# Optimization experiments

Hardware: AMD Instinct MI355X
Metric: run time of the kernel (lower is better)

## Reference

```python
import jax, jax.numpy as jnp
import numpy as np

B, T, F, D, H, DFF, L = 8, 1024, 64, 512, 8, 2048, 3
DH = D // H
PERIODS = np.array([16, 256, 4096], np.int32)
CMS_LRS = np.array([0.01, 0.001, 0.0001], np.float32)
TITANS_LR = 0.01
TITANS_CLIP = 0.1


def layernorm(x, w, b):
    m = x.mean(-1, keepdims=True)
    v = x.var(-1, keepdims=True)
    return (x - m) * jax.lax.rsqrt(v + 1e-5) * w + b


def setup_inputs() -> dict:
    key = jax.random.key(0)
    ks = jax.random.split(key, 40)
    f32 = jnp.float32
    def rn(i, shape, s=0.02):
        return jax.random.normal(ks[i], shape, f32) * s
    inp = {
        'x': jax.random.normal(ks[0], (B, T, F), f32),
        'titans_W': jnp.zeros((D, D), f32),
        'cms_summary': jnp.zeros((L, D), f32),
        'cms_buf_sum': jnp.zeros((L, D), f32),
        'cms_count': jnp.zeros((L,), jnp.int32),
        'cms_step': jnp.zeros((L,), jnp.int32),
        'in_norm_w': jnp.ones((F,), f32), 'in_norm_b': jnp.zeros((F,), f32),
        'in_proj_W': rn(1, (D, F)), 'in_proj_b': jnp.zeros((D,), f32),
        'W_base': rn(2, (D, D), 0.01),
        'tit_out_W': rn(3, (D, D)), 'tit_out_b': jnp.zeros((D,), f32),
        'gate_W': rn(4, (L, D, D)), 'gate_b': jnp.zeros((L, D), f32),
        'comb_W': rn(5, (D, L * D)), 'comb_b': jnp.zeros((D,), f32),
        'n1_w': jnp.ones((D,), f32), 'n1_b': jnp.zeros((D,), f32),
        'qkv_W': rn(6, (3 * D, D)), 'qkv_b': jnp.zeros((3 * D,), f32),
        'ao_W': rn(7, (D, D)), 'ao_b': jnp.zeros((D,), f32),
        'n2_w': jnp.ones((D,), f32), 'n2_b': jnp.zeros((D,), f32),
        'f1_W': rn(8, (DFF, D)), 'f1_b': jnp.zeros((DFF,), f32),
        'f2_W': rn(9, (D, DFF)), 'f2_b': jnp.zeros((D,), f32),
        'fn_w': jnp.ones((D,), f32), 'fn_b': jnp.zeros((D,), f32),
        'head_W': rn(10, (1, D)), 'head_b': jnp.zeros((1,), f32),
    }
    return inp


def cms_tick_all(means, summary, buf_sum, count, step, gate_W, gate_b):
    """Sequential tick over T timesteps, vectorized over the L levels.
    means: [T, D] batch-mean of final hidden at each timestep."""
    periods = jnp.asarray(PERIODS)
    lrs = jnp.asarray(CMS_LRS)
    def step_fn(carry, m):
        summ, bs, cnt, stp = carry
        bs = bs + m[None, :]              # [L, D]
        cnt = cnt + 1
        stp = stp + 1
        fire = cnt >= periods              # [L]
        acc = bs / cnt.astype(bs.dtype)[:, None]
        g = jax.nn.sigmoid(jnp.einsum('lij,lj->li', gate_W, acc) + gate_b)
        new_summ = jnp.where(fire[:, None], (1.0 - lrs)[:, None] * summ + lrs[:, None] * g * acc, summ)
        bs = jnp.where(fire[:, None], jnp.zeros_like(bs), bs)
        cnt = jnp.where(fire, jnp.zeros_like(cnt), cnt)
        return (new_summ, bs, cnt, stp), None
    (summary, buf_sum, count, step), _ = jax.lax.scan(step_fn, (summary, buf_sum, count, step), means)
    return summary, buf_sum, count, step


def reference(x, titans_W, cms_summary, cms_buf_sum, cms_count, cms_step,
              in_norm_w, in_norm_b, in_proj_W, in_proj_b,
              W_base, tit_out_W, tit_out_b,
              gate_W, gate_b, comb_W, comb_b,
              n1_w, n1_b, qkv_W, qkv_b, ao_W, ao_b,
              n2_w, n2_b, f1_W, f1_b, f2_W, f2_b,
              fn_w, fn_b, head_W, head_b):
    # input norm + projection: [B,T,F] -> [B,T,D]
    h = layernorm(x, in_norm_w, in_norm_b) @ in_proj_W.T + in_proj_b
    # Titans fast-weight read
    W = W_base + titans_W
    tit = (h @ W.T) @ tit_out_W.T + tit_out_b
    # Titans fast-weight update (detached in the original)
    hs = jax.lax.stop_gradient(h)
    target = hs.mean(axis=1)               # [B, D]
    query = hs[:, -1, :]                   # [B, D]
    pred_m = query @ titans_W.T
    err = (target - pred_m).mean(axis=0)   # [D]
    grad = jnp.outer(err, query.mean(axis=0))
    gn = jnp.linalg.norm(grad)
    grad = jnp.where(gn > TITANS_CLIP, grad * (TITANS_CLIP / gn), grad)
    new_W = titans_W + TITANS_LR * grad
    h = h + tit
    # CMS residual from current summaries: concat [L*D] -> combine -> [D]
    cms_out = cms_summary.reshape(L * D) @ comb_W.T + comb_b
    h = h + cms_out                        # broadcast over [B,T,D]
    # transformer block (pre-norm, causal MHA)
    hn = layernorm(h, n1_w, n1_b)
    qkv = hn @ qkv_W.T + qkv_b
    q, k, v = jnp.split(qkv, 3, axis=-1)
    def to_heads(t):
        return t.reshape(B, T, H, DH).transpose(0, 2, 1, 3)
    q, k, v = to_heads(q), to_heads(k), to_heads(v)
    scores = jnp.einsum('bhqd,bhkd->bhqk', q, k) / np.sqrt(DH).astype(np.float32)
    causal = jnp.triu(jnp.ones((T, T), bool), 1)
    scores = jnp.where(causal, -jnp.inf, scores)
    attn = jax.nn.softmax(scores, axis=-1)
    ao = jnp.einsum('bhqk,bhkd->bhqd', attn, v).transpose(0, 2, 1, 3).reshape(B, T, D)
    h = h + ao @ ao_W.T + ao_b
    hn2 = layernorm(h, n2_w, n2_b)
    h = h + jax.nn.gelu(hn2 @ f1_W.T + f1_b, approximate=False) @ f2_W.T + f2_b
    h = layernorm(h, fn_w, fn_b)
    pred = (h @ head_W.T + head_b).squeeze(-1)   # [B, T]
    # CMS tick over all T steps (detached in the original)
    means = jax.lax.stop_gradient(h).mean(axis=0)  # [T, D]
    ns, nb, nc, nt = cms_tick_all(means, cms_summary, cms_buf_sum, cms_count, cms_step, gate_W, gate_b)
    return pred, new_W, ns, nb, nc, nt
```

## Files before the change

### kernel.cpp

```cpp
#include <hip/hip_runtime.h>
#include <hip/hip_bf16.h>
#include <math.h>

#define Bdim 8
#define Tdim 1024
#define Fdim 64
#define Ddim 512
#define Lcms 3

#define OFF_PRED 0
#define OFF_W    8192
#define OFF_NS   270336
#define OFF_NB   271872
#define OFF_NC   273408
#define OFF_NT   273411

typedef __hip_bfloat16 bf16;
typedef __attribute__((ext_vector_type(8))) short s8;
typedef __attribute__((ext_vector_type(4))) float f4;

__device__ __forceinline__ float b2f(bf16 v){ return __bfloat162float(v); }
__device__ __forceinline__ bf16  f2b(float v){ return __float2bfloat16(v); }
__device__ __forceinline__ short fb16(float v){ bf16 t = __float2bfloat16(v); return *reinterpret_cast<short*>(&t); }
__device__ __forceinline__ float sh2f(short s){ bf16 t = *reinterpret_cast<bf16*>(&s); return __bfloat162float(t); }
__device__ __forceinline__ float toF(float v){ return v; }
__device__ __forceinline__ float toF(bf16 v){ return __bfloat162float(v); }
template<typename T> __device__ __forceinline__ T fromF(float v);
template<> __device__ __forceinline__ float fromF<float>(float v){ return v; }
template<> __device__ __forceinline__ bf16  fromF<bf16 >(float v){ return f2b(v); }

__device__ __forceinline__ f4 mfma16(s8 a, s8 b, f4 c){
  return __builtin_amdgcn_mfma_f32_16x16x32_bf16(a, b, c, 0, 0, 0);
}

__device__ __forceinline__ void gload16(const bf16* g, bf16* l){
  __builtin_amdgcn_global_load_lds(
      (const __attribute__((address_space(1))) unsigned*)g,
      (__attribute__((address_space(3))) unsigned*)l, 16, 0, 0);
}

__device__ __forceinline__ float gelu_fast(float x){
  float z2 = 1.5957691216f*(x + 0.044715f*x*x*x);
  z2 = fminf(fmaxf(z2, -18.f), 18.f);
  return x / (1.f + __expf(-z2));
}

template<typename TW>
__device__ __forceinline__ void front_misc(int blk, int tid,
    const TW* x, const TW* nw, const TW* nb_, bf16* xn,
    const TW* Wbse, const TW* tW, bf16* Wout,
    const TW* summ, const TW* combW, const TW* combb, float* outv){
  if (blk < 2048){
    int row = blk*4 + (tid>>6);
    int lane = tid & 63;
    float v = toF(x[(size_t)row*Fdim + lane]);
    float s = v, s2 = v*v;
    #pragma unroll
    for (int off=32; off; off>>=1){ s += __shfl_down(s,off); s2 += __shfl_down(s2,off); }
    s = __shfl(s, 0); s2 = __shfl(s2, 0);
    float mu = s*(1.f/64.f);
    float var = s2*(1.f/64.f) - mu*mu;
    float rstd = rsqrtf(var + 1e-5f);
    xn[(size_t)row*Fdim + lane] = f2b((v-mu)*rstd*toF(nw[lane]) + toF(nb_[lane]));
  } else if (blk < 3072){
    int i = (blk-2048)*256 + tid;
    Wout[i] = f2b(toF(Wbse[i]) + toF(tW[i]));
  } else {
    __shared__ float s_s[Lcms*Ddim];
    for (int i=tid;i<Lcms*Ddim;i+=256) s_s[i] = toF(summ[i]);
    __syncthreads();
    int wave = tid>>6, lane = tid&63;
    int d = (blk-3072)*4 + wave;
    const TW* wr = combW + (size_t)d*(Lcms*Ddim);
    float a = 0.f;
    for (int j=lane;j<Lcms*Ddim;j+=64) a += s_s[j]*toF(wr[j]);
    #pragma unroll
    for (int off=32; off; off>>=1) a += __shfl_down(a,off);
    if (lane==0) outv[d] = a + toF(combb[d]);
  }
}
__global__ __launch_bounds__(256) void k_front(
    const void* s0, const void* s1, const void* s2, const void* s3,
    const void* s4, const void* s5, const void* s6, const void* s7,
    const void* s8v, const void* s9, const void* s10, const void* s11,
    const void* s12, const void* s13,
    bf16* __restrict__ dst, const unsigned* __restrict__ w1, int* __restrict__ flag,
    const int* __restrict__ cnt, int* __restrict__ params,
    const void* x, const void* nw, const void* nb_, bf16* xn,
    const void* Wbse, const void* tW, bf16* Wout,
    const void* summ, const void* combW, const void* combb, float* outv,
    float* __restrict__ colsum){
  bool isbf = (w1[0] == 0x3F803F80u);
  int blk = blockIdx.x, tid = threadIdx.x;
  if (blk==0 && tid==0){
    flag[0] = isbf ? 1 : 0;
    const int P[3] = {16,256,4096};
    for (int l=0;l<3;l++){
      int c0 = cnt[l];
      int t1 = P[l] - c0 - 1; if (t1 < 0) t1 = 0;
      int K = (t1 >= Tdim) ? 0 : 1 + (Tdim-1-t1)/P[l];
      params[l*4+0]=t1; params[l*4+1]=K; params[l*4+2]=c0+t1+1; params[l*4+3]=c0;
    }
  }
  if (blk == 1){
    for (int i=tid; i<Bdim*Ddim; i+=256) colsum[i] = 0.f;
  }
  if (blk < 1024){
    const void* srcs[14] = {s0,s1,s2,s3,s4,s5,s6,s7,s8v,s9,s10,s11,s12,s13};
    const int   ns[14]   = {262144,512,786432,1536,262144,512,1048576,2048,1048576,512,
                            32768,512,786432,1536};
    const int gstride = 1024*256;
    int gid = blk*256 + tid;
    int base = 0;
    #pragma unroll
    for (int s=0;s<14;s++){
      int n = ns[s];
      if (isbf){
        const short* sp = (const short*)srcs[s]; short* dp = (short*)(dst+base);
        for (int i=gid;i<n;i+=gstride) dp[i] = sp[i];
      } else {
        const float* sp = (const float*)srcs[s];
        for (int i=gid;i<n;i+=gstride) dst[base+i] = f2b(sp[i]);
      }
      base += n;
    }
  } else {
    int b2 = blk - 1024;
    if (isbf) front_misc<bf16>(b2, tid, (const bf16*)x,(const bf16*)nw,(const bf16*)nb_,xn,
                               (const bf16*)Wbse,(const bf16*)tW,Wout,
                               (const bf16*)summ,(const bf16*)combW,(const bf16*)combb,outv);
    else      front_misc<float>(b2, tid, (const float*)x,(const float*)nw,(const float*)nb_,xn,
                               (const float*)Wbse,(const float*)tW,Wout,
                               (const float*)summ,(const float*)combW,(const float*)combb,outv);
  }
}

template<typename TW>
__device__ __forceinline__ void titans_err_impl(const bf16* h, const float* colsum,
    const TW* tW, float* err, float* qmean){
  int wave = threadIdx.x>>6, lane = threadIdx.x&63;
  int d = blockIdx.x*4 + wave;
  const TW* wr = tW + (size_t)d*Ddim;
  float s = 0.f;
  #pragma unroll
  for (int b=0;b<Bdim;b++){
    const bf16* q = h + ((size_t)b*Tdim + (Tdim-1))*Ddim;
    float p = 0.f;
    for (int j=lane;j<Ddim;j+=64) p += b2f(q[j])*toF(wr[j]);
    s += p;
  }
  #pragma unroll
  for (int off=32; off; off>>=1) s += __shfl_down(s,off);
  if (lane==0){
    float e=0.f, qm=0.f;
    #pragma unroll
    for (int b=0;b<Bdim;b++){
      e  += colsum[b*Ddim+d]*(1.f/(float)Tdim);
      qm += b2f(h[((size_t)b*Tdim + (Tdim-1))*Ddim + d]);
    }
    err[d]   = (e - s)*(1.f/(float)Bdim);
    qmean[d] = qm*(1.f/(float)Bdim);
  }
}
__global__ __launch_bounds__(256) void k_titans_err(const bf16* h, const float* colsum,
    const void* tW, float* err, float* qmean, const int* flg){
  if (*flg) titans_err_impl<bf16>(h,colsum,(const bf16*)tW,err,qmean);
  else      titans_err_impl<float>(h,colsum,(const float*)tW,err,qmean);
}

template<typename TW>
__device__ __forceinline__ void new_W_impl(const TW* tW, const float* err, const float* qmean,
    TW* outW){
  int tid = threadIdx.x;
  float a = err[tid]*err[tid] + err[tid+256]*err[tid+256];
  float b = qmean[tid]*qmean[tid] + qmean[tid+256]*qmean[tid+256];
  #pragma unroll
  for (int off=32; off; off>>=1){ a += __shfl_down(a,off); b += __shfl_down(b,off); }
  __shared__ float sa[4], sb[4];
  int lane = tid & 63, wid = tid >> 6;
  if (lane==0){ sa[wid]=a; sb[wid]=b; }
  __syncthreads();
  float A = sa[0]+sa[1]+sa[2]+sa[3];
  float Bq= sb[0]+sb[1]+sb[2]+sb[3];
  float gn = sqrtf(A*Bq);
  float sf = 0.01f * (gn > 0.1f ? 0.1f/gn : 1.0f);
  int i = blockIdx.x*256 + tid;
  int r = i >> 9, c = i & 511;
  outW[i] = fromF<TW>(toF(tW[i]) + sf*err[r]*qmean[c]);
}
__global__ __launch_bounds__(256) void k_new_W(const void* tW, const float* err,
    const float* qmean, void* out, const int* flg){
  if (*flg) new_W_impl<bf16>((const bf16*)tW, err, qmean, ((bf16*)out)+OFF_W);
  else      new_W_impl<float>((const float*)tW, err, qmean, ((float*)out)+OFF_W);
}

template<int MODE, int DEPTH>
__global__ __launch_bounds__(512) void gemm_mfma(const bf16* __restrict__ A,
    const bf16* __restrict__ Bw, const bf16* __restrict__ bias,
    const float* __restrict__ colvec, bf16* __restrict__ Cout,
    const bf16* __restrict__ resid, int M, int N, int K, float* __restrict__ colsum){
  __shared__ __align__(16) bf16 As[DEPTH][128*32];
  __shared__ __align__(16) bf16 Bs[DEPTH][128*32];
  int tid = threadIdx.x, wave = tid>>6, lane = tid&63, quad = lane>>4, l16 = lane&15;
  int row0 = blockIdx.x*128, col0 = blockIdx.y*128;
  int wr = (wave>>2)*64, wc = (wave&3)*32;
  int srow = wave*16 + (lane>>2);
  int scol = (((lane&3) ^ ((lane>>3)&3)))*8;
  int rswz = (quad ^ ((l16>>1)&3))*8;
  f4 acc[8] = {};
  int niter = K >> 5;
  #define STAGE(bu, k0) { \
    gload16(A  + (size_t)(row0 + srow)*K + (k0) + scol, &As[bu][wave*512 + lane*8]); \
    gload16(Bw + (size_t)(col0 + srow)*K + (k0) + scol, &Bs[bu][wave*512 + lane*8]); \
  }
  STAGE(0, 0)
  if (DEPTH >= 3 && niter > 1) STAGE(1, 32)
  if (DEPTH >= 4 && niter > 2) STAGE(2, 64)
  for (int k=0; k<niter; k++){
    int bu = k & (DEPTH-1);
    if (DEPTH == 2){
      if (k+1 < niter){
        STAGE((k+1)&1, (k+1)<<5)
        asm volatile("s_waitcnt vmcnt(2)" ::: "memory");
      } else {
        asm volatile("s_waitcnt vmcnt(0)" ::: "memory");
      }
    } else {
      if (k+3 < niter){
        STAGE((k+3)&3, (k+3)<<5)
        asm volatile("s_waitcnt vmcnt(6)" ::: "memory");
      } else if (k+2 < niter){
        asm volatile("s_waitcnt vmcnt(4)" ::: "memory");
      } else if (k+1 < niter){
        asm volatile("s_waitcnt vmcnt(2)" ::: "memory");
      } else {
        asm volatile("s_waitcnt vmcnt(0)" ::: "memory");
      }
    }
    __builtin_amdgcn_s_barrier();
    s8 af[4], bfv[2];
    #pragma unroll
    for (int i=0;i<4;i++) af[i]  = *reinterpret_cast<const s8*>(&As[bu][(wr + i*16 + l16)*32 + rswz]);
    #pragma unroll
    for (int j=0;j<2;j++) bfv[j] = *reinterpret_cast<const s8*>(&Bs[bu][(wc + j*16 + l16)*32 + rswz]);
    #pragma unroll
    for (int i=0;i<4;i++)
      #pragma unroll
      for (int j=0;j<2;j++)
        acc[i*2+j] = mfma16(af[i], bfv[j], acc[i*2+j]);
    asm volatile("s_waitcnt lgkmcnt(0)" ::: "memory");
    __builtin_amdgcn_s_barrier();
  }
  #undef STAGE
  float cs[2] = {0.f, 0.f};
  #pragma unroll
  for (int i=0;i<4;i++){
    #pragma unroll
    for (int j=0;j<2;j++){
      int n = col0 + wc + j*16 + l16;
      f4 a = acc[i*2+j];
      #pragma unroll
      for (int r=0;r<4;r++){
        int m = row0 + wr + i*16 + quad*4 + r;
        float v = a[r];
        if (MODE & 1) v += b2f(bias[n]);
        if (MODE & 8) v += colvec[n];
        if (MODE & 4) v = gelu_fast(v);
        if (MODE & 2) v += b2f(resid[(size_t)m*Ddim + n]);
        Cout[(size_t)m*N + n] = f2b(v);
        if (MODE & 16) cs[j] += v;
      }
    }
  }
  if (MODE & 16){
    int bIdx = blockIdx.x >> 3;
    #pragma unroll
    for (int j=0;j<2;j++){
      float c = cs[j];
      c += __shfl_xor(c, 16);
      c += __shfl_xor(c, 32);
      if (quad == 0)
        atomicAdd(&colsum[bIdx*Ddim + col0 + wc + j*16 + l16], c);
    }
  }
}

template<int MODE>
__global__ __launch_bounds__(512) void gemm_mfma64(const bf16* __restrict__ A,
    const bf16* __restrict__ Bw, const bf16* __restrict__ bias,
    const float* __restrict__ colvec, bf16* __restrict__ Cout,
    const bf16* __restrict__ resid, int M, int N, int K){
  __shared__ __align__(16) bf16 As[2][64*32];
  __shared__ __align__(16) bf16 Bs[2][128*32];
  int tid = threadIdx.x, wave = tid>>6, lane = tid&63, quad = lane>>4, l16 = lane&15;
  int row0 = blockIdx.x*64, col0 = blockIdx.y*128;
  int wr = (wave>>2)*32, wc = (wave&3)*32;
  int srow = lane>>2;
  int scol = (((lane&3) ^ ((lane>>3)&3)))*8;
  int rswz = (quad ^ ((l16>>1)&3))*8;
  f4 acc[4] = {};
  int niter = K >> 5;
  #define STAGE64(bu, k0) { \
    if (wave < 4) \
      gload16(A + (size_t)(row0 + wave*16 + srow)*K + (k0) + scol, &As[bu][wave*512 + lane*8]); \
    gload16(Bw + (size_t)(col0 + wave*16 + srow)*K + (k0) + scol, &Bs[bu][wave*512 + lane*8]); \
  }
  STAGE64(0, 0)
  for (int k=0; k<niter; k++){
    int bu = k & 1;
    if (k+1 < niter){
      STAGE64((k+1)&1, (k+1)<<5)
      if (wave < 4) asm volatile("s_waitcnt vmcnt(2)" ::: "memory");
      else          asm volatile("s_waitcnt vmcnt(1)" ::: "memory");
    } else {
      asm volatile("s_waitcnt vmcnt(0)" ::: "memory");
    }
    __builtin_amdgcn_s_barrier();
    s8 af[2], bfv[2];
    #pragma unroll
    for (int i=0;i<2;i++) af[i]  = *reinterpret_cast<const s8*>(&As[bu][(wr + i*16 + l16)*32 + rswz]);
    #pragma unroll
    for (int j=0;j<2;j++) bfv[j] = *reinterpret_cast<const s8*>(&Bs[bu][(wc + j*16 + l16)*32 + rswz]);
    #pragma unroll
    for (int i=0;i<2;i++)
      #pragma unroll
      for (int j=0;j<2;j++)
        acc[i*2+j] = mfma16(af[i], bfv[j], acc[i*2+j]);
    asm volatile("s_waitcnt lgkmcnt(0)" ::: "memory");
    __builtin_amdgcn_s_barrier();
  }
  #undef STAGE64
  #pragma unroll
  for (int i=0;i<2;i++){
    #pragma unroll
    for (int j=0;j<2;j++){
      int n = col0 + wc + j*16 + l16;
      f4 a = acc[i*2+j];
      #pragma unroll
      for (int r=0;r<4;r++){
        int m = row0 + wr + i*16 + quad*4 + r;
        float v = a[r];
        if (MODE & 1) v += b2f(bias[n]);
        if (MODE & 8) v += colvec[n];
        if (MODE & 4) v = gelu_fast(v);
        if (MODE & 2) v += b2f(resid[(size_t)m*Ddim + n]);
        Cout[(size_t)m*N + n] = f2b(v);
      }
    }
  }
}

template<typename TW>
__device__ __forceinline__ void ln_impl(const bf16* in, const TW* w, const TW* b, bf16* outp){
  int row = blockIdx.x;
  const bf16* r = in + (size_t)row*Ddim;
  int tid = threadIdx.x;
  float v0 = b2f(r[tid]), v1 = b2f(r[tid + 256]);
  float s = v0+v1, s2 = v0*v0 + v1*v1;
  #pragma unroll
  for (int off=32; off; off>>=1){ s += __shfl_down(s,off); s2 += __shfl_down(s2,off); }
  __shared__ float sa[4], sb[4];
  int lane = tid & 63, wid = tid >> 6;
  if (lane==0){ sa[wid]=s; sb[wid]=s2; }
  __syncthreads();
  float ts  = sa[0]+sa[1]+sa[2]+sa[3];
  float ts2 = sb[0]+sb[1]+sb[2]+sb[3];
  float mu = ts*(1.f/(float)Ddim);
  float var = ts2*(1.f/(float)Ddim) - mu*mu;
  float rstd = rsqrtf(var + 1e-5f);
  outp[(size_t)row*Ddim + tid]       = f2b((v0-mu)*rstd*toF(w[tid])     + toF(b[tid]));
  outp[(size_t)row*Ddim + tid + 256] = f2b((v1-mu)*rstd*toF(w[tid+256]) + toF(b[tid+256]));
}
__global__ __launch_bounds__(256) void k_ln(const bf16* in, const void* w, const void* b,
    bf16* outp, const int* flg){
  if (*flg) ln_impl<bf16>(in,(const bf16*)w,(const bf16*)b,outp);
  else      ln_impl<float>(in,(const float*)w,(const float*)b,outp);
}

template<typename TW>
__device__ __forceinline__ void ln_hm_impl(const bf16* in, const TW* w, const TW* b,
    bf16* outp, const TW* hw, const TW* hb, TW* pred, float* means){
  int t = blockIdx.x;
  int tid = threadIdx.x, wave = tid>>6, lane = tid&63;
  int d0 = lane*8;
  __shared__ float msum[4][Ddim];
  float wv[8], bv[8], hwv[8];
  #pragma unroll
  for (int j=0;j<8;j++){ wv[j]=toF(w[d0+j]); bv[j]=toF(b[d0+j]); hwv[j]=toF(hw[d0+j]); }
  float hb0 = toF(hb[0]);
  float osum[8] = {0,0,0,0,0,0,0,0};
  #pragma unroll
  for (int rr=0; rr<2; rr++){
    int bb = wave*2 + rr;
    size_t row = (size_t)bb*Tdim + t;
    s8 raw = *reinterpret_cast<const s8*>(in + row*Ddim + d0);
    float v[8];
    float s=0.f, s2=0.f;
    #pragma unroll
    for (int j=0;j<8;j++){ v[j]=sh2f(raw[j]); s+=v[j]; s2+=v[j]*v[j]; }
    #pragma unroll
    for (int off=32; off; off>>=1){ s += __shfl_down(s,off); s2 += __shfl_down(s2,off); }
    s = __shfl(s,0); s2 = __shfl(s2,0);
    float mu = s*(1.f/(float)Ddim);
    float var = s2*(1.f/(float)Ddim) - mu*mu;
    float rstd = rsqrtf(var + 1e-5f);
    float sp = 0.f;
    s8 ob;
    #pragma unroll
    for (int j=0;j<8;j++){
      float o = (v[j]-mu)*rstd*wv[j] + bv[j];
      ob[j] = fb16(o);
      sp += o*hwv[j];
      osum[j] += o;
    }
    *reinterpret_cast<s8*>(outp + row*Ddim + d0) = ob;
    #pragma unroll
    for (int off=32; off; off>>=1) sp += __shfl_down(sp,off);
    if (lane==0) pred[row] = fromF<TW>(sp + hb0);
  }
  #pragma unroll
  for (int j=0;j<8;j++) msum[wave][d0+j] = osum[j];
  __syncthreads();
  for (int d=tid; d<Ddim; d+=256)
    means[(size_t)t*Ddim + d] = (msum[0][d]+msum[1][d]+msum[2][d]+msum[3][d])*(1.f/8.f);
}
__global__ __launch_bounds__(256) void k_ln_hm(const bf16* in, const void* w, const void* b,
    bf16* outp, const void* hw, const void* hb, void* out, float* means, const int* flg){
  if (*flg) ln_hm_impl<bf16>(in,(const bf16*)w,(const bf16*)b,outp,
                             (const bf16*)hw,(const bf16*)hb,((bf16*)out)+OFF_PRED,means);
  else      ln_hm_impl<float>(in,(const float*)w,(const float*)b,outp,
                             (const float*)hw,(const float*)hb,((float*)out)+OFF_PRED,means);
}

__global__ __launch_bounds__(256) void k_attn_mfma(const bf16* __restrict__ qkv,
                                                   bf16* __restrict__ ao){
  int blk = blockIdx.x;
  int bh = blk & 63;
  int qt = 15 - (blk >> 6);
  int head = bh & 7, b = bh >> 3;
  __shared__ __align__(16) bf16 Ks[2][64][72];
  __shared__ __align__(16) unsigned Vt4[2][64*36];
  __shared__ __align__(16) bf16 Ps[4][16][72];
  int tid = threadIdx.x, wave = tid>>6, lane = tid&63, quad = lane>>4, l16 = lane&15;
  int q0w = qt*64 + wave*16;
  const bf16* basep = qkv + (size_t)b*Tdim*1536 + head*64;
  s8 qf0 = *reinterpret_cast<const s8*>(basep + (size_t)(q0w+l16)*1536 + quad*8);
  s8 qf1 = *reinterpret_cast<const s8*>(basep + (size_t)(q0w+l16)*1536 + 32 + quad*8);
  f4 o[4] = {{0,0,0,0},{0,0,0,0},{0,0,0,0},{0,0,0,0}};
  float m_r[4] = {-3.0e38f,-3.0e38f,-3.0e38f,-3.0e38f};
  float l_r[4] = {0.f,0.f,0.f,0.f};
  int key_s = tid>>3, dgk = (tid&7)*8;
  int vp = tid>>3, dgv = (tid&7)*8;
  int vu4 = (((vp>>2) ^ (tid&7)) & 7)*4 + (vp&3);
  int nch = qt + 1;
  s8 kr0[2], kr1[2], vra[2], vrb[2];
  {
    const bf16* kp = basep + (size_t)key_s*1536 + 512 + dgk;
    kr0[0] = *reinterpret_cast<const s8*>(kp);
    kr1[0] = *reinterpret_cast<const s8*>(kp + (size_t)32*1536);
    const bf16* vpa = basep + (size_t)(2*vp)*1536 + 1024 + dgv;
    vra[0] = *reinterpret_cast<const s8*>(vpa);
    vrb[0] = *reinterpret_cast<const s8*>(vpa + 1536);
    if (1 < nch){
      const bf16* kp1 = basep + (size_t)(64+key_s)*1536 + 512 + dgk;
      kr0[1] = *reinterpret_cast<const s8*>(kp1);
      kr1[1] = *reinterpret_cast<const s8*>(kp1 + (size_t)32*1536);
      const bf16* vpa1 = basep + (size_t)(64 + 2*vp)*1536 + 1024 + dgv;
      vra[1] = *reinterpret_cast<const s8*>(vpa1);
      vrb[1] = *reinterpret_cast<const s8*>(vpa1 + 1536);
    }
  }
  auto do_chunk = [&](int ch, int bu){
    f4 sc4[4] = {{0,0,0,0},{0,0,0,0},{0,0,0,0},{0,0,0,0}};
    #pragma unroll
    for (int t=0;t<4;t++){
      sc4[t] = mfma16(qf0, *reinterpret_cast<const s8*>(&Ks[bu][t*16+l16][quad*8]),    sc4[t]);
      sc4[t] = mfma16(qf1, *reinterpret_cast<const s8*>(&Ks[bu][t*16+l16][32+quad*8]), sc4[t]);
    }
    int key0 = ch*64 + l16;
    #pragma unroll
    for (int r=0;r<4;r++){
      int qrow = q0w + quad*4 + r;
      float a0 = (key0      <= qrow) ? sc4[0][r]*0.125f : -3.0e38f;
      float a1 = (key0 + 16 <= qrow) ? sc4[1][r]*0.125f : -3.0e38f;
      float a2 = (key0 + 32 <= qrow) ? sc4[2][r]*0.125f : -3.0e38f;
      float a3 = (key0 + 48 <= qrow) ? sc4[3][r]*0.125f : -3.0e38f;
      float mx = fmaxf(fmaxf(a0,a1), fmaxf(a2,a3));
      mx = fmaxf(mx, __shfl_xor(mx,1)); mx = fmaxf(mx, __shfl_xor(mx,2));
      mx = fmaxf(mx, __shfl_xor(mx,4)); mx = fmaxf(mx, __shfl_xor(mx,8));
      float mnew = fmaxf(m_r[r], mx);
      float al = __expf(m_r[r]-mnew); m_r[r] = mnew;
      float p0 = __expf(a0-mnew), p1 = __expf(a1-mnew);
      float p2 = __expf(a2-mnew), p3 = __expf(a3-mnew);
      float rs = (p0+p1)+(p2+p3);
      rs += __shfl_xor(rs,1); rs += __shfl_xor(rs,2);
      rs += __shfl_xor(rs,4); rs += __shfl_xor(rs,8);
      l_r[r] = l_r[r]*al + rs;
      o[0][r]*=al; o[1][r]*=al; o[2][r]*=al; o[3][r]*=al;
      int prow = quad*4+r;
      *reinterpret_cast<short*>(&Ps[wave][prow][l16])    = fb16(p0);
      *reinterpret_cast<short*>(&Ps[wave][prow][16+l16]) = fb16(p1);
      *reinterpret_cast<short*>(&Ps[wave][prow][32+l16]) = fb16(p2);
      *reinterpret_cast<short*>(&Ps[wave][prow][48+l16]) = fb16(p3);
    }
    asm volatile("s_waitcnt lgkmcnt(0)" ::: "memory");
    s8 pf0 = *reinterpret_cast<const s8*>(&Ps[wave][l16][quad*8]);
    s8 pf1 = *reinterpret_cast<const s8*>(&Ps[wave][l16][32+quad*8]);
    #pragma unroll
    for (int j=0;j<4;j++){
      int d = j*16 + l16;
      int swz = (d>>3) & 7;
      s8 b0 = *reinterpret_cast<const s8*>(&Vt4[bu][d*36 + ((quad   ^ swz))*4]);
      s8 b1 = *reinterpret_cast<const s8*>(&Vt4[bu][d*36 + (((4+quad)^ swz))*4]);
      o[j] = mfma16(pf0, b0, o[j]);
      o[j] = mfma16(pf1, b1, o[j]);
    }
  };
  for (int ch0=0; ch0<nch; ch0+=2){
    #pragma unroll
    for (int s=0;s<2;s++){
      if (ch0+s < nch){
        *reinterpret_cast<s8*>(&Ks[s][key_s][dgk])    = kr0[s];
        *reinterpret_cast<s8*>(&Ks[s][32+key_s][dgk]) = kr1[s];
        #pragma unroll
        for (int j=0;j<8;j++){
          unsigned w = (unsigned)(unsigned short)vra[s][j] | ((unsigned)(unsigned short)vrb[s][j] << 16);
          Vt4[s][(dgv+j)*36 + vu4] = w;
        }
      }
    }
    __syncthreads();
    #pragma unroll
    for (int s=0;s<2;s++){
      int chn = ch0 + 2 + s;
      if (chn < nch){
        const bf16* kp = basep + (size_t)(chn*64+key_s)*1536 + 512 + dgk;
        kr0[s] = *reinterpret_cast<const s8*>(kp);
        kr1[s] = *reinterpret_cast<const s8*>(kp + (size_t)32*1536);
        const bf16* vpa = basep + (size_t)(chn*64 + 2*vp)*1536 + 1024 + dgv;
        vra[s] = *reinterpret_cast<const s8*>(vpa);
        vrb[s] = *reinterpret_cast<const s8*>(vpa + 1536);
      }
    }
    do_chunk(ch0, 0);
    if (ch0+1 < nch) do_chunk(ch0+1, 1);
    if (ch0+2 < nch) __syncthreads();
  }
  #pragma unroll
  for (int r=0;r<4;r++){
    float inv = 1.f/l_r[r];
    size_t rowb = (size_t)(b*Tdim + q0w + quad*4 + r)*Ddim + head*64;
    ao[rowb + l16]      = f2b(o[0][r]*inv);
    ao[rowb + 16 + l16] = f2b(o[1][r]*inv);
    ao[rowb + 32 + l16] = f2b(o[2][r]*inv);
    ao[rowb + 48 + l16] = f2b(o[3][r]*inv);
  }
}

template<typename TW>
__device__ __forceinline__ void cms_acc_impl(const float* means, const TW* bs0,
    const int* params, float* acc, bf16* acch, float* tailtmp){
  int tid = threadIdx.x;
  if (blockIdx.x < 384){
    int l = blockIdx.x>>7, k = blockIdx.x&127;
    int K = params[l*4+1];
    if (k >= K){
      for (int d=tid; d<Ddim; d+=256) acch[((size_t)l*128+k)*Ddim + d] = f2b(0.f);
      return;
    }
    int t1 = params[l*4], cnt0 = params[l*4+2];
    const int P[3] = {16,256,4096};
    int lo = (k==0) ? 0 : t1 + (k-1)*P[l] + 1;
    int hi = t1 + k*P[l];
    float inv = 1.f/((k==0) ? (float)cnt0 : (float)P[l]);
    int lane = tid&63, strip = tid>>6;
    __shared__ float red[4][Ddim];
    float4 a0 = {0,0,0,0}, a1 = {0,0,0,0};
    for (int t=lo+strip; t<=hi; t+=4){
      const float4* row = (const float4*)(means + (size_t)t*Ddim);
      float4 v0 = row[lane], v1 = row[lane+64];
      a0.x+=v0.x; a0.y+=v0.y; a0.z+=v0.z; a0.w+=v0.w;
      a1.x+=v1.x; a1.y+=v1.y; a1.z+=v1.z; a1.w+=v1.w;
    }
    ((float4*)red[strip])[lane]    = a0;
    ((float4*)red[strip])[lane+64] = a1;
    __syncthreads();
    for (int d=tid; d<Ddim; d+=256){
      float s = red[0][d]+red[1][d]+red[2][d]+red[3][d];
      if (k==0) s += toF(bs0[l*Ddim+d]);
      float v = s*inv;
      acc[((size_t)l*65+k)*Ddim + d] = v;
      acch[((size_t)l*128+k)*Ddim + d] = f2b(v);
    }
  } else {
    int bb = blockIdx.x - 384;
    int l = bb>>5, chunk = bb&31;
    int t1 = params[l*4], K = params[l*4+1];
    const int P[3] = {16,256,4096};
    int lo = (K==0) ? 0 : t1 + (K-1)*P[l] + 1;
    int f = tid & 127, strip = tid >> 7;
    int tbeg = chunk*32, tend = tbeg + 32;
    if (tbeg < lo) tbeg = lo;
    float4 a = {0,0,0,0};
    for (int t=tbeg+strip; t<tend; t+=2){
      float4 v = ((const float4*)(means + (size_t)t*Ddim))[f];
      a.x+=v.x; a.y+=v.y; a.z+=v.z; a.w+=v.w;
    }
    __shared__ float4 redt[2][128];
    redt[strip][f] = a;
    __syncthreads();
    if (strip==0){
      float4 b = redt[1][f];
      a.x+=b.x; a.y+=b.y; a.z+=b.z; a.w+=b.w;
      ((float4*)(tailtmp + ((size_t)l*32 + chunk)*Ddim))[f] = a;
    }
  }
}
__global__ __launch_bounds__(256) void k_cms_acc(const float* means, const void* bs0,
    const int* params, float* acc, bf16* acch, float* tailtmp, const int* flg){
  if (*flg) cms_acc_impl<bf16>(means,(const bf16*)bs0,params,acc,acch,tailtmp);
  else      cms_acc_impl<float>(means,(const float*)bs0,params,acc,acch,tailtmp);
}

__global__ __launch_bounds__(256) void k_cms_gate_mfma(const bf16* __restrict__ accbh,
    const bf16* __restrict__ wg, const bf16* __restrict__ wgb, float* __restrict__ g){
  int l = blockIdx.y;
  const bf16* A  = accbh + (size_t)l*128*Ddim;
  const bf16* Bw = wg    + (size_t)l*Ddim*Ddim;
  __shared__ __align__(16) bf16 As[128*32];
  __shared__ __align__(16) bf16 Bs[128*32];
  int tid = threadIdx.x, wave = tid>>6, lane = tid&63, quad = lane>>4, l16 = lane&15;
  int col0 = blockIdx.x*128;
  int wr = (wave>>1)*64, wc = (wave&1)*64;
  int srow = lane>>2, scol = (lane&3)*8;
  f4 acc[16] = {};
  for (int k0=0; k0<Ddim; k0+=32){
    __syncthreads();
    #pragma unroll
    for (int it=0; it<2; it++){
      int c = wave*2 + it;
      gload16(A  + (size_t)(c*16 + srow)*Ddim + k0 + scol, &As[c*512 + lane*8]);
      gload16(Bw + (size_t)(col0 + c*16 + srow)*Ddim + k0 + scol, &Bs[c*512 + lane*8]);
    }
    __syncthreads();
    s8 af[4], bfv[4];
    #pragma unroll
    for (int i=0;i<4;i++) af[i]  = *reinterpret_cast<const s8*>(&As[(wr + i*16 + l16)*32 + quad*8]);
    #pragma unroll
    for (int j=0;j<4;j++) bfv[j] = *reinterpret_cast<const s8*>(&Bs[(wc + j*16 + l16)*32 + quad*8]);
    #pragma unroll
    for (int i=0;i<4;i++)
      #pragma unroll
      for (int j=0;j<4;j++)
        acc[i*4+j] = mfma16(af[i], bfv[j], acc[i*4+j]);
  }
  #pragma unroll
  for (int i=0;i<4;i++){
    #pragma unroll
    for (int j=0;j<4;j++){
      int n = col0 + wc + j*16 + l16;
      f4 a = acc[i*4+j];
      #pragma unroll
      for (int r=0;r<4;r++){
        int m = wr + i*16 + quad*4 + r;
        if (m < 65){
          float v = a[r] + b2f(wgb[l*Ddim + n]);
          g[((size_t)l*65 + m)*Ddim + n] = 1.f/(1.f + __expf(-v));
        }
      }
    }
  }
}

template<typename TW>
__device__ __forceinline__ void cms_final_impl(const float* acc, const float* g,
    const float* tailtmp, const TW* summ0, const TW* bs0, const int* params,
    const int* step0, TW* out){
  int l = blockIdx.x;
  int t1 = params[l*4], K = params[l*4+1], c0 = params[l*4+3];
  const int P[3] = {16,256,4096};
  const float LR[3] = {0.01f,0.001f,0.0001f};
  float lr = LR[l];
  for (int d=threadIdx.x; d<Ddim; d+=256){
    float s = toF(summ0[l*Ddim + d]);
    for (int k=0;k<K;k++)
      s = (1.f-lr)*s + lr*g[((size_t)l*65+k)*Ddim+d]*acc[((size_t)l*65+k)*Ddim+d];
    out[OFF_NS + l*Ddim + d] = fromF<TW>(s);
    float nbv = (K==0) ? toF(bs0[l*Ddim+d]) : 0.f;
    #pragma unroll
    for (int c=0;c<32;c++) nbv += tailtmp[((size_t)l*32+c)*Ddim + d];
    out[OFF_NB + l*Ddim + d] = fromF<TW>(nbv);
  }
  if (threadIdx.x==0){
    int nc = (K==0) ? c0 + Tdim : (Tdim-1 - (t1 + (K-1)*P[l]));
    out[OFF_NC + l] = fromF<TW>((float)nc);
    out[OFF_NT + l] = fromF<TW>((float)(step0[l] + Tdim));
  }
}
__global__ __launch_bounds__(256) void k_cms_final(const float* acc, const float* g,
    const float* tailtmp, const void* summ0, const void* bs0, const int* params,
    const int* step0, void* out, const int* flg){
  if (*flg) cms_final_impl<bf16>(acc,g,tailtmp,(const bf16*)summ0,(const bf16*)bs0,params,step0,(bf16*)out);
  else      cms_final_impl<float>(acc,g,tailtmp,(const float*)summ0,(const float*)bs0,params,step0,(float*)out);
}

extern "C" void kernel_launch(void* const* d_in, const int* in_sizes, int n_in,
                              void* d_out, int out_size, void* d_ws, size_t ws_size,
                              hipStream_t stream) {
  (void)in_sizes; (void)n_in; (void)out_size; (void)ws_size;
  const void* x           = d_in[0];
  const void* titansW     = d_in[1];
  const void* cms_summary = d_in[2];
  const void* cms_bufsum  = d_in[3];
  const int*  cms_count   = (const int*)d_in[4];
  const int*  cms_step    = (const int*)d_in[5];
  const void* in_norm_w   = d_in[6];
  const void* in_norm_b   = d_in[7];
  const void* in_proj_W   = d_in[8];
  const void* in_proj_b   = d_in[9];
  const void* W_base      = d_in[10];
  const void* tit_out_W   = d_in[11];
  const void* tit_out_b   = d_in[12];
  const void* gate_W      = d_in[13];
  const void* gate_b      = d_in[14];
  const void* comb_W      = d_in[15];
  const void* comb_b      = d_in[16];
  const void* n1_w        = d_in[17];
  const void* n1_b        = d_in[18];
  const void* qkv_W       = d_in[19];
  const void* qkv_b       = d_in[20];
  const void* ao_W        = d_in[21];
  const void* ao_b        = d_in[22];
  const void* n2_w        = d_in[23];
  const void* n2_b        = d_in[24];
  const void* f1_W        = d_in[25];
  const void* f1_b        = d_in[26];
  const void* f2_W        = d_in[27];
  const void* f2_b        = d_in[28];
  const void* fn_w        = d_in[29];
  const void* fn_b        = d_in[30];
  const void* head_W      = d_in[31];
  const void* head_b      = d_in[32];

  char* u8 = (char*)d_ws;
  bf16*  h     = (bf16*)(u8 + 0);
  bf16*  hnA   = (bf16*)(u8 + 8388608);
  bf16*  big   = (bf16*)(u8 + 16777216);
  bf16*  xn    = big;
  bf16*  tmid  = big + (size_t)8192*1536;
  float* means = (float*)(u8 + 50331648);
  bf16*  Wb    = (bf16*)(u8 + 52428800);
  bf16*  wall  = (bf16*)(u8 + 52953088);
  bf16*  wtit  = wall;
  bf16*  wtitb = wall + 262144;
  bf16*  wqkv  = wall + 262656;
  bf16*  wqkvb = wall + 1049088;
  bf16*  wao   = wall + 1050624;
  bf16*  waob  = wall + 1312768;
  bf16*  wf1   = wall + 1313280;
  bf16*  wf1b  = wall + 2361856;
  bf16*  wf2   = wall + 2363904;
  bf16*  wf2b  = wall + 3412480;
  bf16*  wproj = wall + 3412992;
  bf16*  wprojb= wall + 3445760;
  bf16*  wgate = wall + 3446272;
  bf16*  wgateb= wall + 4232704;
  float* errv  = (float*)(u8 + 61454336);
  float* qmean = (float*)(u8 + 61456384);
  float* cmsout= (float*)(u8 + 61458944);
  float* accb  = (float*)(u8 + 61460992);
  float* gbuf  = (float*)(u8 + 61860352);
  bf16*  accbh = (bf16*) (u8 + 62259712);
  int*   params= (int*)  (u8 + 62652928);
  int*   dflag = (int*)  (u8 + 62652992);
  float* colsum= (float*)(u8 + 62659584);
  float* tailtmp=(float*)(u8 + 63183872);

  k_front<<<4224, 256, 0, stream>>>(tit_out_W, tit_out_b, qkv_W, qkv_b, ao_W, ao_b,
                                    f1_W, f1_b, f2_W, f2_b, in_proj_W, in_proj_b,
                                    gate_W, gate_b, wall, (const unsigned*)in_norm_w,
                                    dflag, cms_count, params,
                                    x, in_norm_w, in_norm_b, xn,
                                    W_base, titansW, Wb,
                                    cms_summary, comb_W, comb_b, cmsout, colsum);
  gemm_mfma<17,2><<<dim3(64,4), 512, 0, stream>>>(xn, wproj, wprojb, nullptr, h, nullptr, 8192, 512, 64, colsum);
  k_titans_err<<<128, 256, 0, stream>>>(h, colsum, titansW, errv, qmean, dflag);
  k_new_W<<<1024, 256, 0, stream>>>(titansW, errv, qmean, d_out, dflag);
  gemm_mfma64<0><<<dim3(128,4), 512, 0, stream>>>(h, Wb, nullptr, nullptr, tmid, nullptr, 8192, 512, 512);
  gemm_mfma64<11><<<dim3(128,4), 512, 0, stream>>>(tmid, wtit, wtitb, cmsout, h, h, 8192, 512, 512);
  k_ln<<<8192, 256, 0, stream>>>(h, n1_w, n1_b, hnA, dflag);
  gemm_mfma<1,2><<<dim3(64,12), 512, 0, stream>>>(hnA, wqkv, wqkvb, nullptr, big, nullptr, 8192, 1536, 512, nullptr);
  k_attn_mfma<<<1024, 256, 0, stream>>>(big, tmid);
  gemm_mfma64<3><<<dim3(128,4), 512, 0, stream>>>(tmid, wao, waob, nullptr, h, h, 8192, 512, 512);
  k_ln<<<8192, 256, 0, stream>>>(h, n2_w, n2_b, hnA, dflag);
  gemm_mfma<5,2><<<dim3(64,16), 512, 0, stream>>>(hnA, wf1, wf1b, nullptr, big, nullptr, 8192, 2048, 512, nullptr);
  gemm_mfma64<3><<<dim3(128,4), 512, 0, stream>>>(big, wf2, wf2b, nullptr, h, h, 8192, 512, 2048);
  k_ln_hm<<<1024, 256, 0, stream>>>(h, fn_w, fn_b, hnA, head_W, head_b, d_out, means, dflag);
  k_cms_acc<<<480, 256, 0, stream>>>(means, cms_bufsum, params, accb, accbh, tailtmp, dflag);
  k_cms_gate_mfma<<<dim3(4,3), 256, 0, stream>>>(accbh, wgate, wgateb, gbuf);
  k_cms_final<<<Lcms, 256, 0, stream>>>(accb, gbuf, tailtmp, cms_summary, cms_bufsum, params, cms_step, d_out, dflag);
}
```

Before: 419.7 us.

## Fold LayerNorm into following GEMMs via row stats and precomputed weight vectors

Removes the two standalone LayerNorm kernels before the QKV and FFN1 GEMMs. The preceding residual GEMM epilogues now accumulate per-row sum and sum-of-squares with atomics. The LN gain is folded into the weight copies in k_front, which also precomputes the per-column vectors W·w and W·b+bias. The consuming GEMMs then apply the mean and rstd correction in their epilogue to the raw residual stream. This saves two full read/write passes over the activation tensor and two launches, at the cost of atomics, more work in k_front, and precision risk from the E[x²]-μ² variance formula applied to bf16-rounded values.

Measured after the change: 431.8 us. 2.9% more time.

```diff
diff --git a/kernel.cpp b/kernel.cpp
--- a/kernel.cpp
+++ b/kernel.cpp
@@ -49,7 +49,9 @@
 __device__ __forceinline__ void front_misc(int blk, int tid,
     const TW* x, const TW* nw, const TW* nb_, bf16* xn,
     const TW* Wbse, const TW* tW, bf16* Wout,
-    const TW* summ, const TW* combW, const TW* combb, float* outv){
+    const TW* summ, const TW* combW, const TW* combb, float* outv,
+    const TW* qkvW, const TW* qkvb, const TW* f1W, const TW* f1b,
+    const TW* n1w, const TW* n1b, const TW* n2w, const TW* n2b, float* cvec){
   if (blk < 2048){
     int row = blk*4 + (tid>>6);
     int lane = tid & 63;
@@ -65,7 +67,7 @@
   } else if (blk < 3072){
     int i = (blk-2048)*256 + tid;
     Wout[i] = f2b(toF(Wbse[i]) + toF(tW[i]));
-  } else {
+  } else if (blk < 3200){
     __shared__ float s_s[Lcms*Ddim];
     for (int i=tid;i<Lcms*Ddim;i+=256) s_s[i] = toF(summ[i]);
     __syncthreads();
@@ -77,6 +79,27 @@
     #pragma unroll
     for (int off=32; off; off>>=1) a += __shfl_down(a,off);
     if (lane==0) outv[d] = a + toF(combb[d]);
+  } else {
+    int wave = tid>>6, lane = tid&63;
+    int n = (blk-3200)*4 + wave;
+    const TW *wr, *lw, *lb; float bb; float *o1, *o2;
+    if (n < 1536){
+      wr = qkvW + (size_t)n*Ddim; lw = n1w; lb = n1b; bb = toF(qkvb[n]);
+      o1 = cvec + n; o2 = cvec + 1536 + n;
+    } else {
+      int m2 = n - 1536;
+      wr = f1W + (size_t)m2*Ddim; lw = n2w; lb = n2b; bb = toF(f1b[m2]);
+      o1 = cvec + 3072 + m2; o2 = cvec + 5120 + m2;
+    }
+    float a1 = 0.f, a2 = 0.f;
+    for (int j=lane;j<Ddim;j+=64){
+      float wv = toF(wr[j]);
+      a1 += wv*toF(lw[j]);
+      a2 += wv*toF(lb[j]);
+    }
+    #pragma unroll
+    for (int off=32; off; off>>=1){ a1 += __shfl_down(a1,off); a2 += __shfl_down(a2,off); }
+    if (lane==0){ *o1 = a1; *o2 = a2 + bb; }
   }
 }
 __global__ __launch_bounds__(256) void k_front(
@@ -89,7 +112,9 @@
     const void* x, const void* nw, const void* nb_, bf16* xn,
     const void* Wbse, const void* tW, bf16* Wout,
     const void* summ, const void* combW, const void* combb, float* outv,
-    float* __restrict__ colsum){
+    float* __restrict__ colsum,
+    const void* n1w, const void* n1b, const void* n2w, const void* n2b,
+    float* __restrict__ cvec, float* __restrict__ rs1, float* __restrict__ rs2){
   bool isbf = (w1[0] == 0x3F803F80u);
   int blk = blockIdx.x, tid = threadIdx.x;
   if (blk==0 && tid==0){
@@ -105,6 +130,12 @@
   if (blk == 1){
     for (int i=tid; i<Bdim*Ddim; i+=256) colsum[i] = 0.f;
   }
+  if (blk == 2){
+    for (int i=tid; i<2*8192; i+=256) rs1[i] = 0.f;
+  }
+  if (blk == 3){
+    for (int i=tid; i<2*8192; i+=256) rs2[i] = 0.f;
+  }
   if (blk < 1024){
     const void* srcs[14] = {s0,s1,s2,s3,s4,s5,s6,s7,s8v,s9,s10,s11,s12,s13};
     const int   ns[14]   = {262144,512,786432,1536,262144,512,1048576,2048,1048576,512,
@@ -115,12 +146,23 @@
     #pragma unroll
     for (int s=0;s<14;s++){
       int n = ns[s];
+      const void* sc = (s==2) ? n1w : (s==6) ? n2w : nullptr;
       if (isbf){
         const short* sp = (const short*)srcs[s]; short* dp = (short*)(dst+base);
-        for (int i=gid;i<n;i+=gstride) dp[i] = sp[i];
+        if (sc){
+          const short* scp = (const short*)sc;
+          for (int i=gid;i<n;i+=gstride) dp[i] = fb16(sh2f(sp[i]) * sh2f(scp[i&511]));
+        } else {
+          for (int i=gid;i<n;i+=gstride) dp[i] = sp[i];
+        }
       } else {
         const float* sp = (const float*)srcs[s];
-        for (int i=gid;i<n;i+=gstride) dst[base+i] = f2b(sp[i]);
+        if (sc){
+          const float* scp = (const float*)sc;
+          for (int i=gid;i<n;i+=gstride) dst[base+i] = f2b(sp[i]*scp[i&511]);
+        } else {
+          for (int i=gid;i<n;i+=gstride) dst[base+i] = f2b(sp[i]);
+        }
       }
       base += n;
     }
@@ -128,10 +170,14 @@
     int b2 = blk - 1024;
     if (isbf) front_misc<bf16>(b2, tid, (const bf16*)x,(const bf16*)nw,(const bf16*)nb_,xn,
                                (const bf16*)Wbse,(const bf16*)tW,Wout,
-                               (const bf16*)summ,(const bf16*)combW,(const bf16*)combb,outv);
+                               (const bf16*)summ,(const bf16*)combW,(const bf16*)combb,outv,
+                               (const bf16*)s2,(const bf16*)s3,(const bf16*)s6,(const bf16*)s7,
+                               (const bf16*)n1w,(const bf16*)n1b,(const bf16*)n2w,(const bf16*)n2b,cvec);
     else      front_misc<float>(b2, tid, (const float*)x,(const float*)nw,(const float*)nb_,xn,
                                (const float*)Wbse,(const float*)tW,Wout,
-                               (const float*)summ,(const float*)combW,(const float*)combb,outv);
+                               (const float*)summ,(const float*)combW,(const float*)combb,outv,
+                               (const float*)s2,(const float*)s3,(const float*)s6,(const float*)s7,
+                               (const float*)n1w,(const float*)n1b,(const float*)n2w,(const float*)n2b,cvec);
   }
 }
 
@@ -198,7 +244,9 @@
 __global__ __launch_bounds__(512) void gemm_mfma(const bf16* __restrict__ A,
     const bf16* __restrict__ Bw, const bf16* __restrict__ bias,
     const float* __restrict__ colvec, bf16* __restrict__ Cout,
-    const bf16* __restrict__ resid, int M, int N, int K, float* __restrict__ colsum){
+    const bf16* __restrict__ resid, int M, int N, int K, float* __restrict__ colsum,
+    const float* __restrict__ rowstat, const float* __restrict__ c1,
+    const float* __restrict__ c2){
   __shared__ __align__(16) bf16 As[DEPTH][128*32];
   __shared__ __align__(16) bf16 Bs[DEPTH][128*32];
   int tid = threadIdx.x, wave = tid>>6, lane = tid&63, quad = lane>>4, l16 = lane&15;
@@ -253,16 +301,25 @@
   }
   #undef STAGE
   float cs[2] = {0.f, 0.f};
+  float invK = 1.f/(float)K;
   #pragma unroll
   for (int i=0;i<4;i++){
     #pragma unroll
     for (int j=0;j<2;j++){
       int n = col0 + wc + j*16 + l16;
       f4 a = acc[i*2+j];
+      float c1v = 0.f, c2v = 0.f;
+      if (MODE & 32){ c1v = c1[n]; c2v = c2[n]; }
       #pragma unroll
       for (int r=0;r<4;r++){
         int m = row0 + wr + i*16 + quad*4 + r;
         float v = a[r];
+        if (MODE & 32){
+          float sm = rowstat[2*m], sq = rowstat[2*m+1];
+          float mu = sm*invK;
+          float rstd = rsqrtf(sq*invK - mu*mu + 1e-5f);
+          v = rstd*v - rstd*mu*c1v + c2v;
+        }
         if (MODE & 1) v += b2f(bias[n]);
         if (MODE & 8) v += colvec[n];
         if (MODE & 4) v = gelu_fast(v);
@@ -289,7 +346,7 @@
 __global__ __launch_bounds__(512) void gemm_mfma64(const bf16* __restrict__ A,
     const bf16* __restrict__ Bw, const bf16* __restrict__ bias,
     const float* __restrict__ colvec, bf16* __restrict__ Cout,
-    const bf16* __restrict__ resid, int M, int N, int K){
+    const bf16* __restrict__ resid, int M, int N, int K, float* __restrict__ rowstat){
   __shared__ __align__(16) bf16 As[2][64*32];
   __shared__ __align__(16) bf16 Bs[2][128*32];
   int tid = threadIdx.x, wave = tid>>6, lane = tid&63, quad = lane>>4, l16 = lane&15;
@@ -330,6 +387,7 @@
     __builtin_amdgcn_s_barrier();
   }
   #undef STAGE64
+  float rsum[2][4] = {}; float r2sum[2][4] = {};
   #pragma unroll
   for (int i=0;i<2;i++){
     #pragma unroll
@@ -345,36 +403,26 @@
         if (MODE & 4) v = gelu_fast(v);
         if (MODE & 2) v += b2f(resid[(size_t)m*Ddim + n]);
         Cout[(size_t)m*N + n] = f2b(v);
+        if (MODE & 32){ rsum[i][r] += v; r2sum[i][r] += v*v; }
       }
     }
   }
-}
-
-template<typename TW>
-__device__ __forceinline__ void ln_impl(const bf16* in, const TW* w, const TW* b, bf16* outp){
-  int row = blockIdx.x;
-  const bf16* r = in + (size_t)row*Ddim;
-  int tid = threadIdx.x;
-  float v0 = b2f(r[tid]), v1 = b2f(r[tid + 256]);
-  float s = v0+v1, s2 = v0*v0 + v1*v1;
-  #pragma unroll
-  for (int off=32; off; off>>=1){ s += __shfl_down(s,off); s2 += __shfl_down(s2,off); }
-  __shared__ float sa[4], sb[4];
-  int lane = tid & 63, wid = tid >> 6;
-  if (lane==0){ sa[wid]=s; sb[wid]=s2; }
-  __syncthreads();
-  float ts  = sa[0]+sa[1]+sa[2]+sa[3];
-  float ts2 = sb[0]+sb[1]+sb[2]+sb[3];
-  float mu = ts*(1.f/(float)Ddim);
-  float var = ts2*(1.f/(float)Ddim) - mu*mu;
-  float rstd = rsqrtf(var + 1e-5f);
-  outp[(size_t)row*Ddim + tid]       = f2b((v0-mu)*rstd*toF(w[tid])     + toF(b[tid]));
-  outp[(size_t)row*Ddim + tid + 256] = f2b((v1-mu)*rstd*toF(w[tid+256]) + toF(b[tid+256]));
-}
-__global__ __launch_bounds__(256) void k_ln(const bf16* in, const void* w, const void* b,
-    bf16* outp, const int* flg){
-  if (*flg) ln_impl<bf16>(in,(const bf16*)w,(const bf16*)b,outp);
-  else      ln_impl<float>(in,(const float*)w,(const float*)b,outp);
+  if (MODE & 32){
+    #pragma unroll
+    for (int i=0;i<2;i++){
+      #pragma unroll
+      for (int r=0;r<4;r++){
+        float s = rsum[i][r], s2 = r2sum[i][r];
+        #pragma unroll
+        for (int mk=8; mk; mk>>=1){ s += __shfl_xor(s,mk); s2 += __shfl_xor(s2,mk); }
+        if (l16 == 0){
+          int mrow = row0 + wr + i*16 + quad*4 + r;
+          atomicAdd(&rowstat[2*mrow],   s);
+          atomicAdd(&rowstat[2*mrow+1], s2);
+        }
+      }
+    }
+  }
 }
 
 template<typename TW>
@@ -775,26 +823,32 @@
   int*   dflag = (int*)  (u8 + 62652992);
   float* colsum= (float*)(u8 + 62659584);
   float* tailtmp=(float*)(u8 + 63183872);
-
-  k_front<<<4224, 256, 0, stream>>>(tit_out_W, tit_out_b, qkv_W, qkv_b, ao_W, ao_b,
+  float* cvec  = (float*)(u8 + 63380480);
+  float* rs1   = (float*)(u8 + 63409152);
+  float* rs2   = (float*)(u8 + 63474688);
+  float* c1q = cvec, *c2q = cvec+1536, *c1f = cvec+3072, *c2f = cvec+5120;
+
+  k_front<<<5120, 256, 0, stream>>>(tit_out_W, tit_out_b, qkv_W, qkv_b, ao_W, ao_b,
                                     f1_W, f1_b, f2_W, f2_b, in_proj_W, in_proj_b,
                                     gate_W, gate_b, wall, (const unsigned*)in_norm_w,
                                     dflag, cms_count, params,
                                     x, in_norm_w, in_norm_b, xn,
                                     W_base, titansW, Wb,
-                                    cms_summary, comb_W, comb_b, cmsout, colsum);
-  gemm_mfma<17,2><<<dim3(64,4), 512, 0, stream>>>(xn, wproj, wprojb, nullptr, h, nullptr, 8192, 512, 64, colsum);
+                                    cms_summary, comb_W, comb_b, cmsout, colsum,
+                                    n1_w, n1_b, n2_w, n2_b, cvec, rs1, rs2);
+  gemm_mfma<17,2><<<dim3(64,4), 512, 0, stream>>>(xn, wproj, wprojb, nullptr, h, nullptr,
+      8192, 512, 64, colsum, nullptr, nullptr, nullptr);
   k_titans_err<<<128, 256, 0, stream>>>(h, colsum, titansW, errv, qmean, dflag);
   k_new_W<<<1024, 256, 0, stream>>>(titansW, errv, qmean, d_out, dflag);
-  gemm_mfma64<0><<<dim3(128,4), 512, 0, stream>>>(h, Wb, nullptr, nullptr, tmid, nullptr, 8192, 512, 512);
-  gemm_mfma64<11><<<dim3(128,4), 512, 0, stream>>>(tmid, wtit, wtitb, cmsout, h, h, 8192, 512, 512);
-  k_ln<<<8192, 256, 0, stream>>>(h, n1_w, n1_b, hnA, dflag);
-  gemm_mfma<1,2><<<dim3(64,12), 512, 0, stream>>>(hnA, wqkv, wqkvb, nullptr, big, nullptr, 8192, 1536, 512, nullptr);
+  gemm_mfma64<0><<<dim3(128,4), 512, 0, stream>>>(h, Wb, nullptr, nullptr, tmid, nullptr, 8192, 512, 512, nullptr);
+  gemm_mfma64<43><<<dim3(128,4), 512, 0, stream>>>(tmid, wtit, wtitb, cmsout, h, h, 8192, 512, 512, rs1);
+  gemm_mfma<32,2><<<dim3(64,12), 512, 0, stream>>>(h, wqkv, nullptr, nullptr, big, nullptr,
+      8192, 1536, 512, nullptr, rs1, c1q, c2q);
   k_attn_mfma<<<1024, 256, 0, stream>>>(big, tmid);
-  gemm_mfma64<3><<<dim3(128,4), 512, 0, stream>>>(tmid, wao, waob, nullptr, h, h, 8192, 512, 512);
-  k_ln<<<8192, 256, 0, stream>>>(h, n2_w, n2_b, hnA, dflag);
-  gemm_mfma<5,2><<<dim3(64,16), 512, 0, stream>>>(hnA, wf1, wf1b, nullptr, big, nullptr, 8192, 2048, 512, nullptr);
-  gemm_mfma64<3><<<dim3(128,4), 512, 0, stream>>>(big, wf2, wf2b, nullptr, h, h, 8192, 512, 2048);
+  gemm_mfma64<35><<<dim3(128,4), 512, 0, stream>>>(tmid, wao, waob, nullptr, h, h, 8192, 512, 512, rs2);
+  gemm_mfma<36,2><<<dim3(64,16), 512, 0, stream>>>(h, wf1, nullptr, nullptr, big, nullptr,
+      8192, 2048, 512, nullptr, rs2, c1f, c2f);
+  gemm_mfma64<3><<<dim3(128,4), 512, 0, stream>>>(big, wf2, wf2b, nullptr, h, h, 8192, 512, 2048, nullptr);
   k_ln_hm<<<1024, 256, 0, stream>>>(h, fn_w, fn_b, hnA, head_W, head_b, d_out, means, dflag);
   k_cms_acc<<<480, 256, 0, stream>>>(means, cms_bufsum, params, accb, accbh, tailtmp, dflag);
   k_cms_gate_mfma<<<dim3(4,3), 256, 0, stream>>>(accbh, wgate, wgateb, gbuf);
```
